# Optimization experiments

Hardware: AMD Instinct MI355X
Metric: run time of the kernel (lower is better)

The kernel has to match this reference:

```python
import jax, jax.numpy as jnp
import numpy as np

N_NODES = 100000
N_EDGES = 1600000
IN_CH = 64
OUT_CH = 64
NUM_K = 9  # (degree+1)^dim = 3*3 quadratic B-spline taps; equals prod(kernel_size) here


def _quad_basis(v):
    # torch_spline_conv quadratic basis for k_mod in {0,1,2}; v = frac(pseudo*(K-deg)) = pseudo here
    return jnp.stack([0.5 * v * v - v + 0.5,
                      -v * v + v + 0.5,
                      0.5 * v * v], axis=-1)  # [E,3]


def spline_conv(x, src, dst, pseudo, W, root, bias, n_nodes):
    # W: [9, C_in, C_out]; basis B: [E, 9]
    b0 = _quad_basis(pseudo[:, 0])          # [E,3]
    b1 = _quad_basis(pseudo[:, 1])          # [E,3]
    B = (b0[:, :, None] * b1[:, None, :]).reshape(pseudo.shape[0], NUM_K)  # [E,9]
    x_src = x[src]                           # gather [E, C_in]
    msg = B[:, 0:1] * (x_src @ W[0])
    for k in range(1, NUM_K):                # fixed small loop over kernel taps
        msg = msg + B[:, k:k + 1] * (x_src @ W[k])
    out = jax.ops.segment_sum(msg, dst, num_segments=n_nodes)  # scatter-add at targets
    return out + x @ root + bias


def setup_inputs() -> dict:
    key = jax.random.key(0)
    ks = jax.random.split(key, 10)
    x = jax.random.normal(ks[0], (N_NODES, IN_CH), dtype=jnp.float32)
    edge_index = jax.random.randint(ks[1], (2, N_EDGES), 0, N_NODES, dtype=jnp.int64)
    pseudo = jax.random.uniform(ks[2], (N_EDGES, 2), dtype=jnp.float32)
    s1 = 1.0 / np.sqrt(IN_CH * NUM_K)
    s2 = 1.0 / np.sqrt(OUT_CH * NUM_K)
    W1 = jax.random.normal(ks[3], (NUM_K, IN_CH, OUT_CH), dtype=jnp.float32) * s1
    root1 = jax.random.normal(ks[4], (IN_CH, OUT_CH), dtype=jnp.float32) * s1
    b1 = jax.random.normal(ks[5], (OUT_CH,), dtype=jnp.float32) * 0.01
    W2 = jax.random.normal(ks[6], (NUM_K, OUT_CH, OUT_CH), dtype=jnp.float32) * s2
    root2 = jax.random.normal(ks[7], (OUT_CH, OUT_CH), dtype=jnp.float32) * s2
    b2 = jax.random.normal(ks[8], (OUT_CH,), dtype=jnp.float32) * 0.01
    return {"x": x, "edge_index": edge_index, "pseudo": pseudo,
            "W1": W1, "root1": root1, "b1": b1,
            "W2": W2, "root2": root2, "b2": b2}


def reference(x, edge_index, pseudo, W1, root1, b1, W2, root2, b2):
    src, dst = edge_index[0], edge_index[1]  # PyG: aggregate messages at target
    h = jax.nn.relu(spline_conv(x, src, dst, pseudo, W1, root1, b1, N_NODES))
    h = jax.nn.relu(spline_conv(h, src, dst, pseudo, W2, root2, b2, N_NODES))
    return h
```

## Files before the change

kernel.cpp:

```cpp
#include <hip/hip_runtime.h>
#include <stdint.h>

typedef __attribute__((ext_vector_type(8))) short bf16x8;
typedef __attribute__((ext_vector_type(4))) float f32x4;

__device__ __forceinline__ float bf2f(unsigned short u) {
  union { unsigned int i; float f; } x; x.i = ((unsigned int)u) << 16; return x.f;
}
__device__ __forceinline__ unsigned short f2bf(float f) {
  union { float f; unsigned int i; } x; x.f = f;
  unsigned int i = x.i;
  return (unsigned short)((i + 0x7FFFu + ((i >> 16) & 1u)) >> 16);
}
__device__ __forceinline__ float f16lo(unsigned int u) {
  union { unsigned short s; _Float16 h; } x; x.s = (unsigned short)(u & 0xFFFFu);
  return (float)x.h;
}
__device__ __forceinline__ float f16hi(unsigned int u) {
  union { unsigned short s; _Float16 h; } x; x.s = (unsigned short)(u >> 16);
  return (float)x.h;
}
__device__ __forceinline__ unsigned int packf16(float a, float b) {
  union { unsigned short s; _Float16 h; } x, y;
  x.h = (_Float16)a; y.h = (_Float16)b;
  return (unsigned int)x.s | ((unsigned int)y.s << 16);
}


__global__ void count_kernel(const int* __restrict__ ei, int E, int* __restrict__ counts) {
  int e = blockIdx.x * blockDim.x + threadIdx.x;
  if (e < E) atomicAdd(&counts[ei[E + e]], 1);
}

__global__ void scan1_kernel(const int* __restrict__ counts, int n, int* __restrict__ bsum) {
  int i = blockIdx.x * 256 + threadIdx.x;
  int v = (i < n) ? counts[i] : 0;
  int lane = threadIdx.x & 63, w = threadIdx.x >> 6;
  for (int d = 32; d > 0; d >>= 1) v += __shfl_down(v, d, 64);
  __shared__ int ws[4];
  if (lane == 0) ws[w] = v;
  __syncthreads();
  if (threadIdx.x == 0) bsum[blockIdx.x] = ws[0] + ws[1] + ws[2] + ws[3];
}

__global__ void scan2_kernel(int* __restrict__ bsum, int G) {
  int t = threadIdx.x;
  int c = (G + 511) >> 9;
  int lo = min(t * c, G), hi = min(lo + c, G);
  int s = 0;
  for (int i = lo; i < hi; ++i) s += bsum[i];
  int lane = t & 63, w = t >> 6;
  int incl = s;
  for (int d = 1; d < 64; d <<= 1) { int u = __shfl_up(incl, d, 64); if (lane >= d) incl += u; }
  __shared__ int wsum[8];
  if (lane == 63) wsum[w] = incl;
  __syncthreads();
  int wpre = 0;
  for (int i = 0; i < w; ++i) wpre += wsum[i];
  int excl = wpre + incl - s;
  for (int i = lo; i < hi; ++i) { int v = bsum[i]; bsum[i] = excl; excl += v; }
}

__global__ void scan3_kernel(const int* __restrict__ counts, int n, const int* __restrict__ bsum,
                             int* __restrict__ offsets, int* __restrict__ cursor, int total) {
  int i = blockIdx.x * 256 + threadIdx.x;
  int v = (i < n) ? counts[i] : 0;
  int lane = threadIdx.x & 63, w = threadIdx.x >> 6;
  int incl = v;
  for (int d = 1; d < 64; d <<= 1) { int u = __shfl_up(incl, d, 64); if (lane >= d) incl += u; }
  __shared__ int wsum[4];
  if (lane == 63) wsum[w] = incl;
  __syncthreads();
  int pre = bsum[blockIdx.x];
  for (int j = 0; j < w; ++j) pre += wsum[j];
  if (i < n) {
    int excl = pre + incl - v;
    offsets[i] = excl;
    cursor[i] = excl;
  }
  if (i == 0) offsets[n] = total;
}


__global__ void fill_kernel(const int* __restrict__ ei, const float* __restrict__ pseudo,
                            int E, int* __restrict__ cursor, uint4* __restrict__ recs) {
  int e = blockIdx.x * blockDim.x + threadIdx.x;
  if (e >= E) return;
  int d = ei[E + e];
  int s = ei[e];
  float2 uv = ((const float2*)pseudo)[e];
  float u = uv.x, v = uv.y;
  float b0 = 0.5f * u * u - u + 0.5f, b1 = -u * u + u + 0.5f, b2 = 0.5f * u * u;
  float c0 = 0.5f * v * v - v + 0.5f, c1 = -v * v + v + 0.5f, c2 = 0.5f * v * v;
  int p = atomicAdd(&cursor[d], 1);
  uint4 r;
  r.x = (((unsigned int)s) << 7) | ((unsigned int)d & 127u);
  r.y = packf16(b0, b1);
  r.z = packf16(b2, c0);
  r.w = packf16(c1, c2);
  recs[p] = r;
}


__global__ void wconv_kernel(const float* __restrict__ W, const float* __restrict__ root,
                             unsigned short* __restrict__ Wt) {
  int i = blockIdx.x * blockDim.x + threadIdx.x;
  if (i >= 640 * 64) return;
  int co = i / 640, r = i % 640;
  float v = (r < 576) ? W[r * 64 + co] : root[(r - 576) * 64 + co];
  Wt[i] = f2bf(v);
}


__global__ void xconv_kernel(const float4* __restrict__ x4, ushort4* __restrict__ xh4, int n4) {
  int i = blockIdx.x * blockDim.x + threadIdx.x;
  if (i < n4) {
    float4 v = x4[i];
    ushort4 o;
    o.x = f2bf(v.x); o.y = f2bf(v.y); o.z = f2bf(v.z); o.w = f2bf(v.w);
    xh4[i] = o;
  }
}


#define SROW 648

#define GX(R) (*(const unsigned short*)(Xb + ((R).x & 0xFFFFFF80u) + laneB))

#define FLUSHROW(C)                                                \
  {                                                                \
    int rb_ = (C) * SROW + lane;                                   \
    sA[rb_ + 0 * 64] = (short)f2bf(a0);                            \
    sA[rb_ + 1 * 64] = (short)f2bf(a1);                            \
    sA[rb_ + 2 * 64] = (short)f2bf(a2);                            \
    sA[rb_ + 3 * 64] = (short)f2bf(a3);                            \
    sA[rb_ + 4 * 64] = (short)f2bf(a4);                            \
    sA[rb_ + 5 * 64] = (short)f2bf(a5);                            \
    sA[rb_ + 6 * 64] = (short)f2bf(a6);                            \
    sA[rb_ + 7 * 64] = (short)f2bf(a7);                            \
    sA[rb_ + 8 * 64] = (short)f2bf(a8);                            \
    a0 = a1 = a2 = a3 = a4 = a5 = a6 = a7 = a8 = 0.f;              \
  }

#define PROC(R, XU)                                                \
  {                                                                \
    int d_ = __builtin_amdgcn_readfirstlane((R).x) & 15;           \
    if (d_ != cur) { FLUSHROW(cur) cur = d_; }                     \
    float xv = bf2f((unsigned short)(XU));                         \
    float b0 = f16lo((R).y), b1 = f16hi((R).y), b2 = f16lo((R).z); \
    float c0 = f16hi((R).z), c1 = f16lo((R).w), c2 = f16hi((R).w); \
    float t0 = b0 * xv, t1 = b1 * xv, t2 = b2 * xv;                \
    a0 += t0 * c0; a1 += t0 * c1; a2 += t0 * c2;                   \
    a3 += t1 * c0; a4 += t1 * c1; a5 += t1 * c2;                   \
    a6 += t2 * c0; a7 += t2 * c1; a8 += t2 * c2;                   \
  }

template <bool OUTBF16>
__global__ __launch_bounds__(256) void fused_kernel(const int* __restrict__ offsets,
                                                    const uint4* __restrict__ recs,
                                                    const unsigned short* __restrict__ Xh,
                                                    const unsigned short* __restrict__ Wt,
                                                    const float* __restrict__ bias,
                                                    void* __restrict__ outv, int N) {
  __shared__ __align__(16) short sA[16 * SROW];
  int tid = threadIdx.x, w = tid >> 6, lane = tid & 63;
  int nodeBase = blockIdx.x * 16;
  const char* Xb = (const char*)Xh;
  unsigned int laneB = (unsigned int)lane * 2u;

  {
    f32x4 z = {0.f, 0.f, 0.f, 0.f};
    for (int i = tid; i < 16 * 36; i += 256) {
      int r = i / 36, c = i - r * 36;
      *(f32x4*)((char*)sA + r * (SROW * 2) + c * 16) = z;
    }
  }
#pragma unroll
  for (int t = 0; t < 4; ++t) {
    int row = w * 4 + t;
    int n = nodeBase + row;
    if (n < N) sA[row * SROW + 576 + lane] = (short)Xh[(size_t)n * 64 + lane];
  }

  {
    int n0 = nodeBase + w * 4;
    int n1 = min(n0 + 4, N);
    if (n0 < N) {
      int j = __builtin_amdgcn_readfirstlane(offsets[n0]);
      int jEnd = __builtin_amdgcn_readfirstlane(offsets[n1]);
      if (j < jEnd) {
        int last = jEnd - 1;
        float a0 = 0.f, a1 = 0.f, a2 = 0.f, a3 = 0.f, a4 = 0.f,
              a5 = 0.f, a6 = 0.f, a7 = 0.f, a8 = 0.f;
        uint4 rA = recs[j];
        uint4 rB = recs[min(j + 1, last)];
        uint4 rC = recs[min(j + 2, last)];
        unsigned int xA = GX(rA);
        unsigned int xB = GX(rB);
        unsigned int xC;
        int cur = __builtin_amdgcn_readfirstlane(rA.x) & 15;
        for (;;) {
          {
            uint4 rN = recs[min(j + 3, last)];
            xC = GX(rC);
            PROC(rA, xA)
            rA = rN;
            if (++j >= jEnd) break;
          }
          {
            uint4 rN = recs[min(j + 3, last)];
            xA = GX(rA);
            PROC(rB, xB)
            rB = rN;
            if (++j >= jEnd) break;
          }
          {
            uint4 rN = recs[min(j + 3, last)];
            xB = GX(rB);
            PROC(rC, xC)
            rC = rN;
            if (++j >= jEnd) break;
          }
        }
        FLUSHROW(cur)
      }
    }
  }
  __syncthreads();

  {
    int r15 = lane & 15, kg = lane >> 4;
    f32x4 acc = {0.f, 0.f, 0.f, 0.f};
#pragma unroll
    for (int kk = 0; kk < 20; ++kk) {
      int kbase = kk * 32 + kg * 8;
      bf16x8 af = *(const bf16x8*)(&sA[r15 * SROW + kbase]);
      bf16x8 bfr = *(const bf16x8*)(Wt + (size_t)(w * 16 + r15) * 640 + kbase);
      acc = __builtin_amdgcn_mfma_f32_16x16x32_bf16(af, bfr, acc, 0, 0, 0);
    }
    int col = w * 16 + r15;
    float bv = bias[col];
    int row0 = kg * 4;
#pragma unroll
    for (int r = 0; r < 4; ++r) {
      int node = nodeBase + row0 + r;
      if (node < N) {
        float val = fmaxf(acc[r] + bv, 0.f);
        size_t idx = (size_t)node * 64 + col;
        if (OUTBF16) ((unsigned short*)outv)[idx] = f2bf(val);
        else ((float*)outv)[idx] = val;
      }
    }
  }
}


extern "C" void kernel_launch(void* const* d_in, const int* in_sizes, int n_in,
                              void* d_out, int out_size, void* d_ws, size_t ws_size,
                              hipStream_t stream) {
  const float* x = (const float*)d_in[0];
  const int* ei = (const int*)d_in[1];
  const float* pseudo = (const float*)d_in[2];
  const float* W1 = (const float*)d_in[3];
  const float* root1 = (const float*)d_in[4];
  const float* b1 = (const float*)d_in[5];
  const float* W2 = (const float*)d_in[6];
  const float* root2 = (const float*)d_in[7];
  const float* b2 = (const float*)d_in[8];

  const int N = in_sizes[0] / 64;
  const int E = in_sizes[1] / 2;
  const int G = (N + 255) / 256;

  char* p = (char*)d_ws;
  auto carve = [&](size_t bytes) -> void* {
    void* r = (void*)p;
    p += (bytes + 255) & ~(size_t)255;
    return r;
  };
  int* counts = (int*)carve((size_t)N * 4);
  int* offsets = (int*)carve((size_t)(N + 1) * 4);
  int* cursor = (int*)carve((size_t)N * 4);
  int* bsum = (int*)carve((size_t)G * 4);
  uint4* recs = (uint4*)carve((size_t)E * 16);
  unsigned short* Wt1 = (unsigned short*)carve(640 * 64 * 2);
  unsigned short* Wt2 = (unsigned short*)carve(640 * 64 * 2);
  unsigned short* h = (unsigned short*)carve((size_t)N * 64 * 2);
  unsigned short* xh = (unsigned short*)carve((size_t)N * 64 * 2);
  (void)ws_size;

  hipMemsetAsync(counts, 0, (size_t)N * 4, stream);
  count_kernel<<<(E + 255) / 256, 256, 0, stream>>>(ei, E, counts);
  scan1_kernel<<<G, 256, 0, stream>>>(counts, N, bsum);
  scan2_kernel<<<1, 512, 0, stream>>>(bsum, G);
  scan3_kernel<<<G, 256, 0, stream>>>(counts, N, bsum, offsets, cursor, E);
  fill_kernel<<<(E + 255) / 256, 256, 0, stream>>>(ei, pseudo, E, cursor, recs);
  wconv_kernel<<<160, 256, 0, stream>>>(W1, root1, Wt1);
  wconv_kernel<<<160, 256, 0, stream>>>(W2, root2, Wt2);
  xconv_kernel<<<(N * 16 + 255) / 256, 256, 0, stream>>>((const float4*)x, (ushort4*)xh, N * 16);

  int FB = (N + 15) / 16;
  fused_kernel<true><<<FB, 256, 0, stream>>>(offsets, recs, xh, Wt1, b1, (void*)h, N);
  fused_kernel<false><<<FB, 256, 0, stream>>>(offsets, recs, h, Wt2, b2, d_out, N);
}
```

Before: 460.6 us.

## Recast per-node edge aggregation as MFMA matmul over edge chunks

Replaces the per-wave scalar FMA loop that accumulated basis-weighted source features into nine per-tap accumulators with a block-wide formulation. Each 64-edge chunk builds a sparse 144x64 basis-weight matrix in shared memory and a transposed gathered-feature tile, then multiplies them with bf16 MFMA to produce per-node, per-tap aggregates. Edge records are staged into shared memory up front. This adds extra barriers per chunk, a large shared-memory footprint that reduces occupancy, and bf16 rounding of the basis products.

```diff
diff --git a/kernel.cpp b/kernel.cpp
--- a/kernel.cpp
+++ b/kernel.cpp
@@ -124,36 +124,9 @@
 
 
 #define SROW 648
-
-#define GX(R) (*(const unsigned short*)(Xb + ((R).x & 0xFFFFFF80u) + laneB))
-
-#define FLUSHROW(C)                                                \
-  {                                                                \
-    int rb_ = (C) * SROW + lane;                                   \
-    sA[rb_ + 0 * 64] = (short)f2bf(a0);                            \
-    sA[rb_ + 1 * 64] = (short)f2bf(a1);                            \
-    sA[rb_ + 2 * 64] = (short)f2bf(a2);                            \
-    sA[rb_ + 3 * 64] = (short)f2bf(a3);                            \
-    sA[rb_ + 4 * 64] = (short)f2bf(a4);                            \
-    sA[rb_ + 5 * 64] = (short)f2bf(a5);                            \
-    sA[rb_ + 6 * 64] = (short)f2bf(a6);                            \
-    sA[rb_ + 7 * 64] = (short)f2bf(a7);                            \
-    sA[rb_ + 8 * 64] = (short)f2bf(a8);                            \
-    a0 = a1 = a2 = a3 = a4 = a5 = a6 = a7 = a8 = 0.f;              \
-  }
-
-#define PROC(R, XU)                                                \
-  {                                                                \
-    int d_ = __builtin_amdgcn_readfirstlane((R).x) & 15;           \
-    if (d_ != cur) { FLUSHROW(cur) cur = d_; }                     \
-    float xv = bf2f((unsigned short)(XU));                         \
-    float b0 = f16lo((R).y), b1 = f16hi((R).y), b2 = f16lo((R).z); \
-    float c0 = f16hi((R).z), c1 = f16lo((R).w), c2 = f16hi((R).w); \
-    float t0 = b0 * xv, t1 = b1 * xv, t2 = b2 * xv;                \
-    a0 += t0 * c0; a1 += t0 * c1; a2 += t0 * c2;                   \
-    a3 += t1 * c0; a4 += t1 * c1; a5 += t1 * c2;                   \
-    a6 += t2 * c0; a7 += t2 * c1; a8 += t2 * c2;                   \
-  }
+#define MPITCH 72
+#define XPITCH 72
+#define RCAP 512
 
 template <bool OUTBF16>
 __global__ __launch_bounds__(256) void fused_kernel(const int* __restrict__ offsets,
@@ -163,80 +136,140 @@
                                                     const float* __restrict__ bias,
                                                     void* __restrict__ outv, int N) {
   __shared__ __align__(16) short sA[16 * SROW];
+  __shared__ __align__(16) short sM[144 * MPITCH];
+  __shared__ __align__(16) short sXt[64 * XPITCH];
+  __shared__ __align__(16) uint4 sRec[RCAP];
   int tid = threadIdx.x, w = tid >> 6, lane = tid & 63;
+  int r15 = lane & 15, kg = lane >> 4;
   int nodeBase = blockIdx.x * 16;
+  int nTop = min(nodeBase + 16, N);
   const char* Xb = (const char*)Xh;
   unsigned int laneB = (unsigned int)lane * 2u;
 
+  int blockBeg = offsets[nodeBase];
+  int blockEnd = offsets[nTop];
+  int cnt = blockEnd - blockBeg;
+  int stage = min(cnt, RCAP);
+
+  for (int i = tid; i < stage; i += 256) sRec[i] = recs[(size_t)blockBeg + i];
   {
     f32x4 z = {0.f, 0.f, 0.f, 0.f};
-    for (int i = tid; i < 16 * 36; i += 256) {
-      int r = i / 36, c = i - r * 36;
-      *(f32x4*)((char*)sA + r * (SROW * 2) + c * 16) = z;
-    }
+    for (int i = tid; i < 1296; i += 256) ((f32x4*)sM)[i] = z;
   }
 #pragma unroll
   for (int t = 0; t < 4; ++t) {
     int row = w * 4 + t;
     int n = nodeBase + row;
-    if (n < N) sA[row * SROW + 576 + lane] = (short)Xh[(size_t)n * 64 + lane];
-  }
+    sA[row * SROW + 576 + lane] = (n < N) ? (short)Xh[(size_t)n * 64 + lane] : (short)0;
+  }
+  __syncthreads();
+
+  f32x4 acc[3][4];
+#pragma unroll
+  for (int i = 0; i < 3; ++i)
+#pragma unroll
+    for (int j = 0; j < 4; ++j) acc[i][j] = (f32x4){0.f, 0.f, 0.f, 0.f};
+
+  int nc = (cnt + 63) >> 6;
+  for (int cc = 0; cc < nc; ++cc) {
+    int base = cc * 64;
+    {
+      int slot = tid >> 2, q = tid & 3;
+      int idx = base + slot;
+      if (idx < cnt) {
+        uint4 r = (idx < stage) ? sRec[idx] : recs[(size_t)blockBeg + idx];
+        float b0 = f16lo(r.y), b1 = f16hi(r.y), b2 = f16lo(r.z);
+        float c0 = f16hi(r.z), c1 = f16lo(r.w), c2 = f16hi(r.w);
+        int rowb = (int)(r.x & 15u) * 9;
+        short* mp = &sM[slot];
+        if (q == 0) {
+          mp[(rowb + 0) * MPITCH] = (short)f2bf(b0 * c0);
+          mp[(rowb + 4) * MPITCH] = (short)f2bf(b1 * c1);
+          mp[(rowb + 8) * MPITCH] = (short)f2bf(b2 * c2);
+        } else if (q == 1) {
+          mp[(rowb + 1) * MPITCH] = (short)f2bf(b0 * c1);
+          mp[(rowb + 5) * MPITCH] = (short)f2bf(b1 * c2);
+        } else if (q == 2) {
+          mp[(rowb + 2) * MPITCH] = (short)f2bf(b0 * c2);
+          mp[(rowb + 6) * MPITCH] = (short)f2bf(b2 * c0);
+        } else {
+          mp[(rowb + 3) * MPITCH] = (short)f2bf(b1 * c0);
+          mp[(rowb + 7) * MPITCH] = (short)f2bf(b2 * c1);
+        }
+      }
+    }
+    {
+      unsigned int rx[16];
+#pragma unroll
+      for (int si = 0; si < 16; ++si) {
+        int idx = base + w * 16 + si;
+        rx[si] = (idx < cnt) ? ((idx < stage) ? sRec[idx].x
+                                              : recs[(size_t)blockBeg + idx].x)
+                             : 0xFFFFFFFFu;
+      }
+      unsigned short xv[16];
+#pragma unroll
+      for (int si = 0; si < 16; ++si)
+        xv[si] = (rx[si] != 0xFFFFFFFFu)
+                     ? *(const unsigned short*)(Xb + (rx[si] & 0xFFFFFF80u) + laneB)
+                     : (unsigned short)0;
+#pragma unroll
+      for (int si = 0; si < 16; ++si)
+        sXt[lane * XPITCH + w * 16 + si] = (short)xv[si];
+    }
+    __syncthreads();
+    {
+      bf16x8 bf[4][2];
+#pragma unroll
+      for (int ct = 0; ct < 4; ++ct)
+#pragma unroll
+        for (int ks = 0; ks < 2; ++ks)
+          bf[ct][ks] = *(const bf16x8*)&sXt[(ct * 16 + r15) * XPITCH + kg * 8 + ks * 32];
+      f32x4 z = {0.f, 0.f, 0.f, 0.f};
+#pragma unroll
+      for (int rti = 0; rti < 3; ++rti) {
+        int rt = w + rti * 4;
+        if (rt < 9) {
+          bf16x8 a0 = *(const bf16x8*)&sM[(rt * 16 + r15) * MPITCH + kg * 8];
+          bf16x8 a1 = *(const bf16x8*)&sM[(rt * 16 + r15) * MPITCH + kg * 8 + 32];
+#pragma unroll
+          for (int ct = 0; ct < 4; ++ct) {
+            acc[rti][ct] = __builtin_amdgcn_mfma_f32_16x16x32_bf16(a0, bf[ct][0], acc[rti][ct], 0, 0, 0);
+            acc[rti][ct] = __builtin_amdgcn_mfma_f32_16x16x32_bf16(a1, bf[ct][1], acc[rti][ct], 0, 0, 0);
+          }
+          for (int i = lane; i < 144; i += 64)
+            *(f32x4*)((char*)sM + rt * 2304 + i * 16) = z;
+        }
+      }
+    }
+    __syncthreads();
+  }
+
+#pragma unroll
+  for (int rti = 0; rti < 3; ++rti) {
+    int rt = w + rti * 4;
+    if (rt < 9) {
+#pragma unroll
+      for (int r = 0; r < 4; ++r) {
+        int rowout = rt * 16 + kg * 4 + r;
+        int n = rowout / 9;
+        int kk = rowout - n * 9;
+#pragma unroll
+        for (int ct = 0; ct < 4; ++ct)
+          sA[n * SROW + kk * 64 + ct * 16 + r15] = (short)f2bf(acc[rti][ct][r]);
+      }
+    }
+  }
+  __syncthreads();
 
   {
-    int n0 = nodeBase + w * 4;
-    int n1 = min(n0 + 4, N);
-    if (n0 < N) {
-      int j = __builtin_amdgcn_readfirstlane(offsets[n0]);
-      int jEnd = __builtin_amdgcn_readfirstlane(offsets[n1]);
-      if (j < jEnd) {
-        int last = jEnd - 1;
-        float a0 = 0.f, a1 = 0.f, a2 = 0.f, a3 = 0.f, a4 = 0.f,
-              a5 = 0.f, a6 = 0.f, a7 = 0.f, a8 = 0.f;
-        uint4 rA = recs[j];
-        uint4 rB = recs[min(j + 1, last)];
-        uint4 rC = recs[min(j + 2, last)];
-        unsigned int xA = GX(rA);
-        unsigned int xB = GX(rB);
-        unsigned int xC;
-        int cur = __builtin_amdgcn_readfirstlane(rA.x) & 15;
-        for (;;) {
-          {
-            uint4 rN = recs[min(j + 3, last)];
-            xC = GX(rC);
-            PROC(rA, xA)
-            rA = rN;
-            if (++j >= jEnd) break;
-          }
-          {
-            uint4 rN = recs[min(j + 3, last)];
-            xA = GX(rA);
-            PROC(rB, xB)
-            rB = rN;
-            if (++j >= jEnd) break;
-          }
-          {
-            uint4 rN = recs[min(j + 3, last)];
-            xB = GX(rB);
-            PROC(rC, xC)
-            rC = rN;
-            if (++j >= jEnd) break;
-          }
-        }
-        FLUSHROW(cur)
-      }
-    }
-  }
-  __syncthreads();
-
-  {
-    int r15 = lane & 15, kg = lane >> 4;
-    f32x4 acc = {0.f, 0.f, 0.f, 0.f};
+    f32x4 oacc = {0.f, 0.f, 0.f, 0.f};
 #pragma unroll
     for (int kk = 0; kk < 20; ++kk) {
       int kbase = kk * 32 + kg * 8;
       bf16x8 af = *(const bf16x8*)(&sA[r15 * SROW + kbase]);
       bf16x8 bfr = *(const bf16x8*)(Wt + (size_t)(w * 16 + r15) * 640 + kbase);
-      acc = __builtin_amdgcn_mfma_f32_16x16x32_bf16(af, bfr, acc, 0, 0, 0);
+      oacc = __builtin_amdgcn_mfma_f32_16x16x32_bf16(af, bfr, oacc, 0, 0, 0);
     }
     int col = w * 16 + r15;
     float bv = bias[col];
@@ -245,7 +278,7 @@
     for (int r = 0; r < 4; ++r) {
       int node = nodeBase + row0 + r;
       if (node < N) {
-        float val = fmaxf(acc[r] + bv, 0.f);
+        float val = fmaxf(oacc[r] + bv, 0.f);
         size_t idx = (size_t)node * 64 + col;
         if (OUTBF16) ((unsigned short*)outv)[idx] = f2bf(val);
         else ((float*)outv)[idx] = val;
```

Result: slower. 747.8 us (+62.4%).
